# Kernel tuning notes

Hardware: AMD Instinct MI355X
Metric: run time of the kernel (lower is better)

Reference implementation:

```python
import jax, jax.numpy as jnp
import numpy as np

NSITES = 64   # 2 * nphysical spin-orbital sites
BOND = 128    # MPS bond dimension D
BATCH = 16384 # sampled occupation configurations


def setup_inputs() -> dict:
    key = jax.random.key(0)
    k1, k2, k3, k4 = jax.random.split(key, 4)
    # Site tensors A[k, n] in R^{D x D}; scaled so chain products stay O(1).
    data = jax.random.normal(k1, (NSITES, 2, BOND, BOND), dtype=jnp.float32) / jnp.sqrt(jnp.float32(BOND))
    left = jax.random.normal(k2, (BOND,), dtype=jnp.float32)
    right = jax.random.normal(k3, (BOND,), dtype=jnp.float32)
    # Occupation-number vectors (0/1 per spin orbital).
    onstate = jax.random.randint(k4, (BATCH, NSITES), 0, 2, dtype=jnp.int32)
    # Orbital-ordering permutation (identity here).
    image2 = jnp.arange(NSITES, dtype=jnp.int32)
    return {"onstate": onstate, "data": data, "left": left, "right": right, "image2": image2}


def reference(onstate, data, left, right, image2):
    # Reorder physical indices per the stored orbital image: [B, NSITES]
    occ = onstate[:, image2]
    B = occ.shape[0]
    D = left.shape[0]
    v0 = jnp.broadcast_to(left, (B, D))  # left boundary, batched

    def step(v, xs):
        A, n = xs  # A: [2, D, D] site tensor, n: [B] occupations at this site
        # Contract with both quantum-number blocks, then select per sample
        # (equivalent to gathering the block indexed by the occupation).
        v_new = jnp.where((n == 1)[:, None], v @ A[1], v @ A[0])  # [B, D]
        return v_new, None

    vT, _ = jax.lax.scan(step, v0, (data, occ.T))
    return vT @ right  # amplitudes psi(n): [B]
```

## Files before the change

### kernel.cpp

```cpp
#include <hip/hip_runtime.h>
#include <hip/hip_bf16.h>

#define NS 64
#define DIM 128
#define BATCH_N 16384

typedef float f32x4 __attribute__((ext_vector_type(4)));
typedef _Float16 f16x8 __attribute__((ext_vector_type(8)));
typedef unsigned int u32;
typedef unsigned long long u64;

__device__ __forceinline__ unsigned short f2h(float f) {
    _Float16 h = (_Float16)f;
    return __builtin_bit_cast(unsigned short, h);
}

__global__ void prep_frags(const float* __restrict__ data,
                           unsigned short* __restrict__ afrag) {
    int idx = blockIdx.x * blockDim.x + threadIdx.x;
    if (idx >= 64 * 2 * 4 * 8 * 64) return;
    int l  = idx & 63;
    int mm = (idx >> 6) & 7;
    int kk = (idx >> 9) & 3;
    int t  = (idx >> 11) & 1;
    int s  = idx >> 12;
    int m = mm * 16 + (l & 15);
    int kbase = kk * 32 + (l >> 4) * 8;
    const float* a0 = data + ((size_t)s * 2 + 0) * DIM * DIM;
    const float* a1 = a0 + DIM * DIM;
    unsigned short outv[8];
#pragma unroll
    for (int j = 0; j < 8; ++j) {
        int k = kbase + j;
        float v0 = a0[k * DIM + m];
        float vv = (t == 0) ? v0 : (a1[k * DIM + m] - v0);
        outv[j] = f2h(vv);
    }
    *reinterpret_cast<uint4*>(afrag + (size_t)idx * 8) =
        *reinterpret_cast<uint4*>(outv);
}

__global__ void prep_bits(const int* __restrict__ onstate,
                          const int* __restrict__ image2,
                          u64* __restrict__ bits) {
    int r = blockIdx.x * blockDim.x + threadIdx.x;
    if (r >= BATCH_N) return;
    const int* row = onstate + (size_t)r * NS;
    u64 b = 0;
#pragma unroll 8
    for (int t = 0; t < NS; ++t) {
        b |= ((u64)(row[image2[t]] & 1)) << t;
    }
    bits[r] = b;
}

__global__ __launch_bounds__(512, 2)
void mps_main(const unsigned short* __restrict__ afrag,
              const u64* __restrict__ occbits,
              const float* __restrict__ left,
              const float* __restrict__ right,
              float* __restrict__ out) {
    __shared__ unsigned short vlds[2][64 * DIM];
    __shared__ float red[64][33];

    const int tid  = threadIdx.x;
    const int wid  = tid >> 6;
    const int lane = tid & 63;
    const int li   = lane & 15;
    const int g    = lane >> 4;
    const int rbase = blockIdx.x * 64;

    u64 bits[4];
#pragma unroll
    for (int rg = 0; rg < 4; ++rg)
        bits[rg] = occbits[rbase + rg * 16 + li];

    for (int c = tid; c < 64 * 16; c += 512) {
        int r  = c >> 4;
        int kc = c & 15;
        unsigned short tmp[8];
#pragma unroll
        for (int j = 0; j < 8; ++j) tmp[j] = f2h(left[kc * 8 + j]);
        u32 byte = (u32)(r * 256 + kc * 16) ^ ((u32)(r & 7) << 4);
        *reinterpret_cast<uint4*>(reinterpret_cast<char*>(&vlds[0][0]) + byte) =
            *reinterpret_cast<uint4*>(tmp);
    }
    __syncthreads();

    const f16x8 zf = {0, 0, 0, 0, 0, 0, 0, 0};

    f16x8 fa0[4], fd0[4], fa1[4], fd1[4];

#define ISSUE(FA, FD, S_)                                                     \
    {                                                                         \
        const unsigned short* sb_ = afrag + (size_t)(S_) * 32768;             \
        _Pragma("unroll")                                                     \
        for (int kk = 0; kk < 4; ++kk) {                                      \
            FA[kk] = *reinterpret_cast<const f16x8*>(                         \
                sb_ + ((size_t)((0 * 4 + kk) * 8 + wid) * 512) + lane * 8);   \
            FD[kk] = *reinterpret_cast<const f16x8*>(                         \
                sb_ + ((size_t)((1 * 4 + kk) * 8 + wid) * 512) + lane * 8);   \
        }                                                                     \
    }

#define COMPUTE(S_, FA, FD)                                                   \
    {                                                                         \
        const int s_ = (S_);                                                  \
        const char* vb = reinterpret_cast<const char*>(&vlds[s_ & 1][0]);     \
        char*       wb = reinterpret_cast<char*>(&vlds[(s_ + 1) & 1][0]);     \
        f32x4 acc[4];                                                         \
        _Pragma("unroll")                                                     \
        for (int rg = 0; rg < 4; ++rg) acc[rg] = (f32x4){0.f, 0.f, 0.f, 0.f}; \
        f16x8 bfr[4][4];                                                      \
        _Pragma("unroll")                                                     \
        for (int kk = 0; kk < 4; ++kk)                                        \
            _Pragma("unroll")                                                 \
            for (int rg = 0; rg < 4; ++rg) {                                  \
                int r = rg * 16 + li;                                         \
                u32 byte = (u32)(r * 256 + kk * 64 + g * 16) ^                \
                           ((u32)(r & 7) << 4);                               \
                bfr[rg][kk] = *reinterpret_cast<const f16x8*>(vb + byte);     \
            }                                                                 \
        _Pragma("unroll")                                                     \
        for (int kk = 0; kk < 4; ++kk) {                                      \
            _Pragma("unroll")                                                 \
            for (int rg = 0; rg < 4; ++rg) {                                  \
                bool mk = (bits[rg] >> s_) & 1;                               \
                f16x8 mb = mk ? bfr[rg][kk] : zf;                             \
                acc[rg] = __builtin_amdgcn_mfma_f32_16x16x32_f16(             \
                    FA[kk], bfr[rg][kk], acc[rg], 0, 0, 0);                   \
                acc[rg] = __builtin_amdgcn_mfma_f32_16x16x32_f16(             \
                    FD[kk], mb, acc[rg], 0, 0, 0);                            \
            }                                                                 \
        }                                                                     \
        if (s_ < NS - 1) {                                                    \
            _Pragma("unroll")                                                 \
            for (int rg = 0; rg < 4; ++rg) {                                  \
                int r = rg * 16 + li;                                         \
                int mbase = wid * 16 + g * 4;                                 \
                u32 lo = ((u32)f2h(acc[rg][1]) << 16) | f2h(acc[rg][0]);      \
                u32 hi = ((u32)f2h(acc[rg][3]) << 16) | f2h(acc[rg][2]);      \
                u32 byte = (u32)(r * 256 + mbase * 2) ^ ((u32)(r & 7) << 4);  \
                uint2 w = {lo, hi};                                           \
                *reinterpret_cast<uint2*>(wb + byte) = w;                     \
            }                                                                 \
            __syncthreads();                                                  \
        } else {                                                              \
            _Pragma("unroll")                                                 \
            for (int rg = 0; rg < 4; ++rg) {                                  \
                int mbase = wid * 16 + g * 4;                                 \
                const float4 rv =                                             \
                    *reinterpret_cast<const float4*>(right + mbase);          \
                float p = acc[rg][0] * rv.x + acc[rg][1] * rv.y +             \
                          acc[rg][2] * rv.z + acc[rg][3] * rv.w;              \
                red[rg * 16 + li][wid * 4 + g] = p;                           \
            }                                                                 \
            __syncthreads();                                                  \
            if (tid < 64) {                                                   \
                float ssum = 0.f;                                             \
                _Pragma("unroll")                                             \
                for (int i = 0; i < 32; ++i) ssum += red[tid][i];             \
                out[rbase + tid] = ssum;                                      \
            }                                                                 \
        }                                                                     \
    }

    ISSUE(fa0, fd0, 0);
    for (int sp = 0; sp < NS; sp += 2) {
        ISSUE(fa1, fd1, sp + 1);
        COMPUTE(sp, fa0, fd0);
        if (sp + 2 < NS) ISSUE(fa0, fd0, sp + 2);
        COMPUTE(sp + 1, fa1, fd1);
    }

#undef ISSUE
#undef COMPUTE
}

extern "C" void kernel_launch(void* const* d_in, const int* in_sizes, int n_in,
                              void* d_out, int out_size, void* d_ws, size_t ws_size,
                              hipStream_t stream) {
    const int*   onstate = (const int*)d_in[0];
    const float* data    = (const float*)d_in[1];
    const float* left    = (const float*)d_in[2];
    const float* right   = (const float*)d_in[3];
    const int*   image2  = (const int*)d_in[4];
    float* out = (float*)d_out;

    unsigned short* afrag = (unsigned short*)d_ws;
    u64* bits = (u64*)((char*)d_ws + (size_t)2097152 * sizeof(unsigned short));

    prep_frags<<<1024, 256, 0, stream>>>(data, afrag);
    prep_bits<<<64, 256, 0, stream>>>(onstate, image2, bits);
    mps_main<<<256, 512, 0, stream>>>(afrag, bits, left, right, out);
}
```

Measured before the change: 103.9 us.

## Retile wave work to 2 M-tiles by 2 row-groups to cut LDS reads

Each of the 8 waves now owns 2 output column tiles and 2 row groups (32 rows) instead of 1 column tile and all 64 rows. Per-wave LDS reads of the state vector are halved, while register-held A fragments double, since each wave now loads two M-tiles per site. Swizzled LDS read and write offsets are precomputed once, and the final reduction shrinks to 16 partials. The cost is higher VGPR pressure from the doubled fragment buffers, which could hurt occupancy under launch_bounds(512,2).

```diff
diff --git a/kernel.cpp b/kernel.cpp
--- a/kernel.cpp
+++ b/kernel.cpp
@@ -61,19 +61,41 @@
               const float* __restrict__ right,
               float* __restrict__ out) {
     __shared__ unsigned short vlds[2][64 * DIM];
-    __shared__ float red[64][33];
+    __shared__ float red[64][17];
 
     const int tid  = threadIdx.x;
     const int wid  = tid >> 6;
     const int lane = tid & 63;
     const int li   = lane & 15;
     const int g    = lane >> 4;
+    const int mt   = wid >> 1;
+    const int rh   = wid & 1;
     const int rbase = blockIdx.x * 64;
 
-    u64 bits[4];
-#pragma unroll
-    for (int rg = 0; rg < 4; ++rg)
-        bits[rg] = occbits[rbase + rg * 16 + li];
+    u64 bits[2];
+#pragma unroll
+    for (int rr = 0; rr < 2; ++rr)
+        bits[rr] = occbits[rbase + rh * 32 + rr * 16 + li];
+
+    u32 rdoff[2][4];
+#pragma unroll
+    for (int rr = 0; rr < 2; ++rr)
+#pragma unroll
+        for (int kk = 0; kk < 4; ++kk) {
+            int r = rh * 32 + rr * 16 + li;
+            rdoff[rr][kk] =
+                (u32)(r * 256 + kk * 64 + g * 16) ^ ((u32)(r & 7) << 4);
+        }
+    u32 wroff[2][2];
+#pragma unroll
+    for (int mm = 0; mm < 2; ++mm)
+#pragma unroll
+        for (int rr = 0; rr < 2; ++rr) {
+            int r = rh * 32 + rr * 16 + li;
+            int mcol = (mt * 2 + mm) * 16 + g * 4;
+            wroff[mm][rr] =
+                (u32)(r * 256 + mcol * 2) ^ ((u32)(r & 7) << 4);
+        }
 
     for (int c = tid; c < 64 * 16; c += 512) {
         int r  = c >> 4;
@@ -89,88 +111,100 @@
 
     const f16x8 zf = {0, 0, 0, 0, 0, 0, 0, 0};
 
-    f16x8 fa0[4], fd0[4], fa1[4], fd1[4];
-
-#define ISSUE(FA, FD, S_)                                                     \
+    f16x8 fa[2][2][4], fd[2][2][4];
+
+#define ISSUE(BUF, S_)                                                        \
     {                                                                         \
         const unsigned short* sb_ = afrag + (size_t)(S_) * 32768;             \
         _Pragma("unroll")                                                     \
-        for (int kk = 0; kk < 4; ++kk) {                                      \
-            FA[kk] = *reinterpret_cast<const f16x8*>(                         \
-                sb_ + ((size_t)((0 * 4 + kk) * 8 + wid) * 512) + lane * 8);   \
-            FD[kk] = *reinterpret_cast<const f16x8*>(                         \
-                sb_ + ((size_t)((1 * 4 + kk) * 8 + wid) * 512) + lane * 8);   \
-        }                                                                     \
-    }
-
-#define COMPUTE(S_, FA, FD)                                                   \
+        for (int mm = 0; mm < 2; ++mm)                                        \
+            _Pragma("unroll")                                                 \
+            for (int kk = 0; kk < 4; ++kk) {                                  \
+                fa[BUF][mm][kk] = *reinterpret_cast<const f16x8*>(            \
+                    sb_ + ((size_t)((0 * 4 + kk) * 8 + mt * 2 + mm) * 512) +  \
+                    lane * 8);                                                \
+                fd[BUF][mm][kk] = *reinterpret_cast<const f16x8*>(            \
+                    sb_ + ((size_t)((1 * 4 + kk) * 8 + mt * 2 + mm) * 512) +  \
+                    lane * 8);                                                \
+            }                                                                 \
+    }
+
+#define COMPUTE(S_, BUF)                                                      \
     {                                                                         \
         const int s_ = (S_);                                                  \
         const char* vb = reinterpret_cast<const char*>(&vlds[s_ & 1][0]);     \
         char*       wb = reinterpret_cast<char*>(&vlds[(s_ + 1) & 1][0]);     \
-        f32x4 acc[4];                                                         \
-        _Pragma("unroll")                                                     \
-        for (int rg = 0; rg < 4; ++rg) acc[rg] = (f32x4){0.f, 0.f, 0.f, 0.f}; \
-        f16x8 bfr[4][4];                                                      \
+        f32x4 acc[2][2];                                                      \
+        _Pragma("unroll")                                                     \
+        for (int mm = 0; mm < 2; ++mm)                                        \
+            _Pragma("unroll")                                                 \
+            for (int rr = 0; rr < 2; ++rr)                                    \
+                acc[mm][rr] = (f32x4){0.f, 0.f, 0.f, 0.f};                    \
+        f16x8 bfr[2][4];                                                      \
         _Pragma("unroll")                                                     \
         for (int kk = 0; kk < 4; ++kk)                                        \
             _Pragma("unroll")                                                 \
-            for (int rg = 0; rg < 4; ++rg) {                                  \
-                int r = rg * 16 + li;                                         \
-                u32 byte = (u32)(r * 256 + kk * 64 + g * 16) ^                \
-                           ((u32)(r & 7) << 4);                               \
-                bfr[rg][kk] = *reinterpret_cast<const f16x8*>(vb + byte);     \
-            }                                                                 \
+            for (int rr = 0; rr < 2; ++rr)                                    \
+                bfr[rr][kk] =                                                 \
+                    *reinterpret_cast<const f16x8*>(vb + rdoff[rr][kk]);      \
         _Pragma("unroll")                                                     \
         for (int kk = 0; kk < 4; ++kk) {                                      \
             _Pragma("unroll")                                                 \
-            for (int rg = 0; rg < 4; ++rg) {                                  \
-                bool mk = (bits[rg] >> s_) & 1;                               \
-                f16x8 mb = mk ? bfr[rg][kk] : zf;                             \
-                acc[rg] = __builtin_amdgcn_mfma_f32_16x16x32_f16(             \
-                    FA[kk], bfr[rg][kk], acc[rg], 0, 0, 0);                   \
-                acc[rg] = __builtin_amdgcn_mfma_f32_16x16x32_f16(             \
-                    FD[kk], mb, acc[rg], 0, 0, 0);                            \
+            for (int rr = 0; rr < 2; ++rr) {                                  \
+                bool mk = (bits[rr] >> s_) & 1;                               \
+                f16x8 mb = mk ? bfr[rr][kk] : zf;                             \
+                _Pragma("unroll")                                             \
+                for (int mm = 0; mm < 2; ++mm) {                              \
+                    acc[mm][rr] = __builtin_amdgcn_mfma_f32_16x16x32_f16(     \
+                        fa[BUF][mm][kk], bfr[rr][kk], acc[mm][rr], 0, 0, 0);  \
+                    acc[mm][rr] = __builtin_amdgcn_mfma_f32_16x16x32_f16(     \
+                        fd[BUF][mm][kk], mb, acc[mm][rr], 0, 0, 0);           \
+                }                                                             \
             }                                                                 \
         }                                                                     \
         if (s_ < NS - 1) {                                                    \
             _Pragma("unroll")                                                 \
-            for (int rg = 0; rg < 4; ++rg) {                                  \
-                int r = rg * 16 + li;                                         \
-                int mbase = wid * 16 + g * 4;                                 \
-                u32 lo = ((u32)f2h(acc[rg][1]) << 16) | f2h(acc[rg][0]);      \
-                u32 hi = ((u32)f2h(acc[rg][3]) << 16) | f2h(acc[rg][2]);      \
-                u32 byte = (u32)(r * 256 + mbase * 2) ^ ((u32)(r & 7) << 4);  \
-                uint2 w = {lo, hi};                                           \
-                *reinterpret_cast<uint2*>(wb + byte) = w;                     \
-            }                                                                 \
+            for (int mm = 0; mm < 2; ++mm)                                    \
+                _Pragma("unroll")                                             \
+                for (int rr = 0; rr < 2; ++rr) {                              \
+                    u32 lo = ((u32)f2h(acc[mm][rr][1]) << 16) |               \
+                             f2h(acc[mm][rr][0]);                             \
+                    u32 hi = ((u32)f2h(acc[mm][rr][3]) << 16) |               \
+                             f2h(acc[mm][rr][2]);                             \
+                    uint2 w = {lo, hi};                                       \
+                    *reinterpret_cast<uint2*>(wb + wroff[mm][rr]) = w;        \
+                }                                                             \
             __syncthreads();                                                  \
         } else {                                                              \
             _Pragma("unroll")                                                 \
-            for (int rg = 0; rg < 4; ++rg) {                                  \
-                int mbase = wid * 16 + g * 4;                                 \
-                const float4 rv =                                             \
-                    *reinterpret_cast<const float4*>(right + mbase);          \
-                float p = acc[rg][0] * rv.x + acc[rg][1] * rv.y +             \
-                          acc[rg][2] * rv.z + acc[rg][3] * rv.w;              \
-                red[rg * 16 + li][wid * 4 + g] = p;                           \
+            for (int rr = 0; rr < 2; ++rr) {                                  \
+                float p = 0.f;                                                \
+                _Pragma("unroll")                                             \
+                for (int mm = 0; mm < 2; ++mm) {                              \
+                    int mcol = (mt * 2 + mm) * 16 + g * 4;                    \
+                    const float4 rv =                                         \
+                        *reinterpret_cast<const float4*>(right + mcol);       \
+                    p += acc[mm][rr][0] * rv.x + acc[mm][rr][1] * rv.y +      \
+                         acc[mm][rr][2] * rv.z + acc[mm][rr][3] * rv.w;       \
+                }                                                             \
+                red[rh * 32 + rr * 16 + li][mt * 4 + g] = p;                  \
             }                                                                 \
             __syncthreads();                                                  \
             if (tid < 64) {                                                   \
                 float ssum = 0.f;                                             \
                 _Pragma("unroll")                                             \
-                for (int i = 0; i < 32; ++i) ssum += red[tid][i];             \
+                for (int i = 0; i < 16; ++i) ssum += red[tid][i];             \
                 out[rbase + tid] = ssum;                                      \
             }                                                                 \
         }                                                                     \
     }
 
-    ISSUE(fa0, fd0, 0);
+    ISSUE(0, 0);
     for (int sp = 0; sp < NS; sp += 2) {
-        ISSUE(fa1, fd1, sp + 1);
-        COMPUTE(sp, fa0, fd0);
-        if (sp + 2 < NS) ISSUE(fa0, fd0, sp + 2);
-        COMPUTE(sp + 1, fa1, fd1);
+        ISSUE(1, sp + 1);
+        COMPUTE(sp, 0);
+        if (sp + 2 < NS) ISSUE(0, sp + 2);
+        COMPUTE(sp + 1, 1);
     }
 
 #undef ISSUE
```

Result: no change. 105.9 us (+1.9%).

## Pair adjacent MPS sites into precomputed product tensors to halve serial steps

Applied to the files above, without the earlier changes.

Precomputes, for each pair of adjacent sites, the four product matrices A0B0, (A1-A0)B0, A0(B1-B0) and (A1-A0)(B1-B0) in a new prep kernel. The main kernel then takes 32 paired steps instead of 64 single ones, each doing four masked MFMAs per k-chunk, which halves the barriers and LDS round trips on the serial chain. The cost is a heavier prep GEMM kernel run on only 128 blocks, twice the fragment registers, and fp16 rounding of products whose values may grow. It also precomputes LDS offsets and raises wave priority around the MFMA section.

```diff
diff --git a/kernel.cpp b/kernel.cpp
--- a/kernel.cpp
+++ b/kernel.cpp
@@ -2,6 +2,7 @@
 #include <hip/hip_bf16.h>
 
 #define NS 64
+#define NP 32
 #define DIM 128
 #define BATCH_N 16384
 
@@ -15,29 +16,91 @@
     return __builtin_bit_cast(unsigned short, h);
 }
 
-__global__ void prep_frags(const float* __restrict__ data,
-                           unsigned short* __restrict__ afrag) {
-    int idx = blockIdx.x * blockDim.x + threadIdx.x;
-    if (idx >= 64 * 2 * 4 * 8 * 64) return;
-    int l  = idx & 63;
-    int mm = (idx >> 6) & 7;
-    int kk = (idx >> 9) & 3;
-    int t  = (idx >> 11) & 1;
-    int s  = idx >> 12;
-    int m = mm * 16 + (l & 15);
-    int kbase = kk * 32 + (l >> 4) * 8;
-    const float* a0 = data + ((size_t)s * 2 + 0) * DIM * DIM;
-    const float* a1 = a0 + DIM * DIM;
-    unsigned short outv[8];
-#pragma unroll
-    for (int j = 0; j < 8; ++j) {
-        int k = kbase + j;
-        float v0 = a0[k * DIM + m];
-        float vv = (t == 0) ? v0 : (a1[k * DIM + m] - v0);
-        outv[j] = f2h(vv);
-    }
-    *reinterpret_cast<uint4*>(afrag + (size_t)idx * 8) =
-        *reinterpret_cast<uint4*>(outv);
+__global__ __launch_bounds__(256)
+void prep_pair_frags(const float* __restrict__ data,
+                     unsigned short* __restrict__ afrag) {
+    __shared__ float LA[2 * 32 * 129];
+    __shared__ float LB[2 * 32 * 128];
+
+    const int p   = blockIdx.x >> 2;
+    const int kk  = blockIdx.x & 3;
+    const int tid = threadIdx.x;
+    const int kgrp = tid >> 5;
+    const int mgrp = tid & 31;
+
+    const float* A0 = data + ((size_t)(2 * p) * 2 + 0) * DIM * DIM;
+    const float* A1 = A0 + DIM * DIM;
+    const float* B0 = data + ((size_t)(2 * p + 1) * 2 + 0) * DIM * DIM;
+    const float* B1 = B0 + DIM * DIM;
+
+    for (int c = tid; c < 32 * DIM; c += 256) {
+        int kl = c >> 7, j = c & 127;
+        float a0 = A0[(kk * 32 + kl) * DIM + j];
+        float a1 = A1[(kk * 32 + kl) * DIM + j];
+        LA[kl * 129 + j] = a0;
+        LA[32 * 129 + kl * 129 + j] = a1 - a0;
+    }
+
+    float acc[2][2][4][4];
+#pragma unroll
+    for (int L = 0; L < 2; ++L)
+#pragma unroll
+        for (int R = 0; R < 2; ++R)
+#pragma unroll
+            for (int i = 0; i < 4; ++i)
+#pragma unroll
+                for (int mi = 0; mi < 4; ++mi) acc[L][R][i][mi] = 0.f;
+
+    for (int ch = 0; ch < 4; ++ch) {
+        __syncthreads();
+        for (int c = tid; c < 32 * DIM; c += 256) {
+            int jl = c >> 7, m = c & 127;
+            float b0 = B0[(ch * 32 + jl) * DIM + m];
+            float b1 = B1[(ch * 32 + jl) * DIM + m];
+            LB[jl * 128 + m] = b0;
+            LB[4096 + jl * 128 + m] = b1 - b0;
+        }
+        __syncthreads();
+#pragma unroll 2
+        for (int jl = 0; jl < 32; ++jl) {
+            int j = ch * 32 + jl;
+            float la0[4], la1[4];
+#pragma unroll
+            for (int i = 0; i < 4; ++i) {
+                la0[i] = LA[(kgrp * 4 + i) * 129 + j];
+                la1[i] = LA[32 * 129 + (kgrp * 4 + i) * 129 + j];
+            }
+            f32x4 lb0 = *reinterpret_cast<const f32x4*>(&LB[jl * 128 + mgrp * 4]);
+            f32x4 lb1 = *reinterpret_cast<const f32x4*>(&LB[4096 + jl * 128 + mgrp * 4]);
+#pragma unroll
+            for (int i = 0; i < 4; ++i)
+#pragma unroll
+                for (int mi = 0; mi < 4; ++mi) {
+                    acc[0][0][i][mi] += la0[i] * lb0[mi];
+                    acc[1][0][i][mi] += la1[i] * lb0[mi];
+                    acc[0][1][i][mi] += la0[i] * lb1[mi];
+                    acc[1][1][i][mi] += la1[i] * lb1[mi];
+                }
+        }
+    }
+
+#pragma unroll
+    for (int t = 0; t < 4; ++t) {
+        int L = t & 1, R = t >> 1;
+#pragma unroll
+        for (int i = 0; i < 4; ++i)
+#pragma unroll
+            for (int mi = 0; mi < 4; ++mi) {
+                int k = kk * 32 + kgrp * 4 + i;
+                int m = mgrp * 4 + mi;
+                int g = (k & 31) >> 3, j = k & 7;
+                int lane = g * 16 + (m & 15);
+                int mm = m >> 4;
+                size_t idx =
+                    ((((((size_t)p * 4 + t) * 4 + kk) * 8 + mm) * 64 + lane) * 8) + j;
+                afrag[idx] = f2h(acc[L][R][i][mi]);
+            }
+    }
 }
 
 __global__ void prep_bits(const int* __restrict__ onstate,
@@ -55,7 +118,7 @@
 }
 
 __global__ __launch_bounds__(512, 2)
-void mps_main(const unsigned short* __restrict__ afrag,
+void mps_pair(const unsigned short* __restrict__ afrag,
               const u64* __restrict__ occbits,
               const float* __restrict__ left,
               const float* __restrict__ right,
@@ -75,6 +138,23 @@
     for (int rg = 0; rg < 4; ++rg)
         bits[rg] = occbits[rbase + rg * 16 + li];
 
+    u32 rdoff[4][4];
+#pragma unroll
+    for (int rg = 0; rg < 4; ++rg)
+#pragma unroll
+        for (int kk = 0; kk < 4; ++kk) {
+            int r = rg * 16 + li;
+            rdoff[rg][kk] =
+                (u32)(r * 256 + kk * 64 + g * 16) ^ ((u32)(r & 7) << 4);
+        }
+    u32 wroff[4];
+#pragma unroll
+    for (int rg = 0; rg < 4; ++rg) {
+        int r = rg * 16 + li;
+        int mbase = wid * 16 + g * 4;
+        wroff[rg] = (u32)(r * 256 + mbase * 2) ^ ((u32)(r & 7) << 4);
+    }
+
     for (int c = tid; c < 64 * 16; c += 512) {
         int r  = c >> 4;
         int kc = c & 15;
@@ -89,71 +169,71 @@
 
     const f16x8 zf = {0, 0, 0, 0, 0, 0, 0, 0};
 
-    f16x8 fa0[4], fd0[4], fa1[4], fd1[4];
-
-#define ISSUE(FA, FD, S_)                                                     \
+    f16x8 ft[2][4][4];
+
+#define ISSUE(BUF, P_)                                                        \
     {                                                                         \
-        const unsigned short* sb_ = afrag + (size_t)(S_) * 32768;             \
+        const unsigned short* sb_ = afrag + (size_t)(P_) * 65536;             \
         _Pragma("unroll")                                                     \
-        for (int kk = 0; kk < 4; ++kk) {                                      \
-            FA[kk] = *reinterpret_cast<const f16x8*>(                         \
-                sb_ + ((size_t)((0 * 4 + kk) * 8 + wid) * 512) + lane * 8);   \
-            FD[kk] = *reinterpret_cast<const f16x8*>(                         \
-                sb_ + ((size_t)((1 * 4 + kk) * 8 + wid) * 512) + lane * 8);   \
-        }                                                                     \
-    }
-
-#define COMPUTE(S_, FA, FD)                                                   \
+        for (int t = 0; t < 4; ++t)                                           \
+            _Pragma("unroll")                                                 \
+            for (int kk = 0; kk < 4; ++kk)                                    \
+                ft[BUF][t][kk] = *reinterpret_cast<const f16x8*>(             \
+                    sb_ + ((size_t)((t * 4 + kk) * 8 + wid) * 512) +          \
+                    lane * 8);                                                \
+    }
+
+#define COMPUTE(P_, BUF)                                                      \
     {                                                                         \
-        const int s_ = (S_);                                                  \
-        const char* vb = reinterpret_cast<const char*>(&vlds[s_ & 1][0]);     \
-        char*       wb = reinterpret_cast<char*>(&vlds[(s_ + 1) & 1][0]);     \
+        const int p_ = (P_);                                                  \
+        const char* vb = reinterpret_cast<const char*>(&vlds[p_ & 1][0]);     \
+        char*       wb = reinterpret_cast<char*>(&vlds[(p_ + 1) & 1][0]);     \
         f32x4 acc[4];                                                         \
         _Pragma("unroll")                                                     \
         for (int rg = 0; rg < 4; ++rg) acc[rg] = (f32x4){0.f, 0.f, 0.f, 0.f}; \
-        f16x8 bfr[4][4];                                                      \
-        _Pragma("unroll")                                                     \
-        for (int kk = 0; kk < 4; ++kk)                                        \
-            _Pragma("unroll")                                                 \
-            for (int rg = 0; rg < 4; ++rg) {                                  \
-                int r = rg * 16 + li;                                         \
-                u32 byte = (u32)(r * 256 + kk * 64 + g * 16) ^                \
-                           ((u32)(r & 7) << 4);                               \
-                bfr[rg][kk] = *reinterpret_cast<const f16x8*>(vb + byte);     \
-            }                                                                 \
+        __builtin_amdgcn_s_setprio(1);                                        \
         _Pragma("unroll")                                                     \
         for (int kk = 0; kk < 4; ++kk) {                                      \
+            f16x8 bfr[4];                                                     \
+            _Pragma("unroll")                                                 \
+            for (int rg = 0; rg < 4; ++rg)                                    \
+                bfr[rg] =                                                     \
+                    *reinterpret_cast<const f16x8*>(vb + rdoff[rg][kk]);      \
             _Pragma("unroll")                                                 \
             for (int rg = 0; rg < 4; ++rg) {                                  \
-                bool mk = (bits[rg] >> s_) & 1;                               \
-                f16x8 mb = mk ? bfr[rg][kk] : zf;                             \
-                acc[rg] = __builtin_amdgcn_mfma_f32_16x16x32_f16(             \
-                    FA[kk], bfr[rg][kk], acc[rg], 0, 0, 0);                   \
-                acc[rg] = __builtin_amdgcn_mfma_f32_16x16x32_f16(             \
-                    FD[kk], mb, acc[rg], 0, 0, 0);                            \
+                bool m0 = (bits[rg] >> (2 * p_)) & 1;                         \
+                bool m1 = (bits[rg] >> (2 * p_ + 1)) & 1;                     \
+                f16x8 vb0  = m0 ? bfr[rg] : zf;                               \
+                f16x8 vb1  = m1 ? bfr[rg] : zf;                               \
+                f16x8 vb01 = m1 ? vb0 : zf;                                   \
+                acc[rg] = __builtin_amdgcn_mfma_f32_16x16x32_f16(             \
+                    ft[BUF][0][kk], bfr[rg], acc[rg], 0, 0, 0);               \
+                acc[rg] = __builtin_amdgcn_mfma_f32_16x16x32_f16(             \
+                    ft[BUF][1][kk], vb0, acc[rg], 0, 0, 0);                   \
+                acc[rg] = __builtin_amdgcn_mfma_f32_16x16x32_f16(             \
+                    ft[BUF][2][kk], vb1, acc[rg], 0, 0, 0);                   \
+                acc[rg] = __builtin_amdgcn_mfma_f32_16x16x32_f16(             \
+                    ft[BUF][3][kk], vb01, acc[rg], 0, 0, 0);                  \
             }                                                                 \
         }                                                                     \
-        if (s_ < NS - 1) {                                                    \
+        __builtin_amdgcn_s_setprio(0);                                        \
+        if (p_ < NP - 1) {                                                    \
             _Pragma("unroll")                                                 \
             for (int rg = 0; rg < 4; ++rg) {                                  \
-                int r = rg * 16 + li;                                         \
-                int mbase = wid * 16 + g * 4;                                 \
                 u32 lo = ((u32)f2h(acc[rg][1]) << 16) | f2h(acc[rg][0]);      \
                 u32 hi = ((u32)f2h(acc[rg][3]) << 16) | f2h(acc[rg][2]);      \
-                u32 byte = (u32)(r * 256 + mbase * 2) ^ ((u32)(r & 7) << 4);  \
                 uint2 w = {lo, hi};                                           \
-                *reinterpret_cast<uint2*>(wb + byte) = w;                     \
+                *reinterpret_cast<uint2*>(wb + wroff[rg]) = w;                \
             }                                                                 \
             __syncthreads();                                                  \
         } else {                                                              \
+            int mcol = wid * 16 + g * 4;                                      \
+            const float4 rv = *reinterpret_cast<const float4*>(right + mcol); \
             _Pragma("unroll")                                                 \
             for (int rg = 0; rg < 4; ++rg) {                                  \
-                int mbase = wid * 16 + g * 4;                                 \
-                const float4 rv =                                             \
-                    *reinterpret_cast<const float4*>(right + mbase);          \
-                float p = acc[rg][0] * rv.x + acc[rg][1] * rv.y +             \
-                          acc[rg][2] * rv.z + acc[rg][3] * rv.w;              \
-                red[rg * 16 + li][wid * 4 + g] = p;                           \
+                float pv = acc[rg][0] * rv.x + acc[rg][1] * rv.y +            \
+                           acc[rg][2] * rv.z + acc[rg][3] * rv.w;             \
+                red[rg * 16 + li][wid * 4 + g] = pv;                          \
             }                                                                 \
             __syncthreads();                                                  \
             if (tid < 64) {                                                   \
@@ -165,12 +245,12 @@
         }                                                                     \
     }
 
-    ISSUE(fa0, fd0, 0);
-    for (int sp = 0; sp < NS; sp += 2) {
-        ISSUE(fa1, fd1, sp + 1);
-        COMPUTE(sp, fa0, fd0);
-        if (sp + 2 < NS) ISSUE(fa0, fd0, sp + 2);
-        COMPUTE(sp + 1, fa1, fd1);
+    ISSUE(0, 0);
+    for (int pp = 0; pp < NP; pp += 2) {
+        ISSUE(1, pp + 1);
+        COMPUTE(pp, 0);
+        if (pp + 2 < NP) ISSUE(0, pp + 2);
+        COMPUTE(pp + 1, 1);
     }
 
 #undef ISSUE
@@ -190,7 +270,7 @@
     unsigned short* afrag = (unsigned short*)d_ws;
     u64* bits = (u64*)((char*)d_ws + (size_t)2097152 * sizeof(unsigned short));
 
-    prep_frags<<<1024, 256, 0, stream>>>(data, afrag);
+    prep_pair_frags<<<128, 256, 0, stream>>>(data, afrag);
     prep_bits<<<64, 256, 0, stream>>>(onstate, image2, bits);
-    mps_main<<<256, 512, 0, stream>>>(afrag, bits, left, right, out);
-}
+    mps_pair<<<256, 512, 0, stream>>>(afrag, bits, left, right, out);
+}
```

Result: slower. 113.4 us (+9.1%).
